# Kernel optimization log

Measured on AMD Instinct MI355X. Metric: run time of the kernel, lower is better.

## Reference

```python
import jax, jax.numpy as jnp
import numpy as np

N_NODES = 8192
N_EDGES = 524288
D_IN = 256
D_OUT = 256


def setup_inputs() -> dict:
    key = jax.random.key(0)
    ks = jax.random.split(key, 8)
    h = jax.random.normal(ks[0], (N_NODES, D_IN), dtype=jnp.float32)
    # Xavier-uniform-like scale for weights
    s = (6.0 / (D_IN + D_OUT)) ** 0.5
    W = jax.random.uniform(ks[1], (D_IN, D_OUT), jnp.float32, -s, s)
    Wq = jax.random.uniform(ks[2], (D_IN, D_OUT), jnp.float32, -s, s)
    bq = jnp.zeros((D_OUT,), jnp.float32)
    Wk = jax.random.uniform(ks[3], (D_IN, D_OUT), jnp.float32, -s, s)
    bk = jnp.zeros((D_OUT,), jnp.float32)
    senders = jax.random.randint(ks[4], (N_EDGES,), 0, N_NODES, dtype=jnp.int64 if jax.config.jax_enable_x64 else jnp.int32)
    receivers = jax.random.randint(ks[5], (N_EDGES,), 0, N_NODES, dtype=jnp.int64 if jax.config.jax_enable_x64 else jnp.int32)
    return {"h": h, "W": W, "Wq": Wq, "bq": bq, "Wk": Wk, "bk": bk,
            "senders": senders, "receivers": receivers}


def reference(h, W, Wq, bq, Wk, bk, senders, receivers):
    # Projected node features: (N, D_OUT)
    h_proj = jnp.dot(h, W)
    # Dense attention logits a = q @ k^T: (N, N), as in the original module
    q = jnp.dot(h, Wq) + bq
    k = jnp.dot(h, Wk) + bk
    a = jnp.dot(q, k.T)
    # Gather per-edge messages and attention weights, weight, scatter-add
    messages = h_proj[senders] * a[senders, receivers][:, None]  # (E, D_OUT)
    aggregated = jax.ops.segment_sum(messages, receivers, num_segments=h.shape[0])
    return jax.nn.relu(aggregated)
```

## Files before the change

kernel.cpp:

```cpp
#include <hip/hip_runtime.h>
#include <stdint.h>

typedef unsigned short u16;
typedef unsigned int u32;
typedef short v8s __attribute__((ext_vector_type(8)));
typedef float v4f __attribute__((ext_vector_type(4)));

#define N_NODES 8192
#define N_EDGES 524288
#define DFEAT 256
#define PAD 160

static __device__ __forceinline__ float bflo(u32 u) { return __uint_as_float(u << 16); }
static __device__ __forceinline__ float bfhi(u32 u) { return __uint_as_float(u & 0xffff0000u); }
static __device__ __forceinline__ u16 f2bf(float f) {
    u32 u = __float_as_uint(f);
    u32 r = (u + 0x7fffu + ((u >> 16) & 1u)) >> 16;
    return (u16)r;
}

__global__ void conv_h(const float* __restrict__ h, u16* __restrict__ hb) {
    int i = (blockIdx.x * 256 + threadIdx.x) * 4;
    float4 v = *(const float4*)(h + i);
    uint2 p;
    p.x = (u32)f2bf(v.x) | ((u32)f2bf(v.y) << 16);
    p.y = (u32)f2bf(v.z) | ((u32)f2bf(v.w) << 16);
    *(uint2*)(hb + i) = p;
}

__global__ void transpose_w(const float* __restrict__ w0, const float* __restrict__ w1,
                            const float* __restrict__ w2, u16* __restrict__ wt) {
    __shared__ u16 t[64][65];
    int b = blockIdx.x;
    int region = b >> 4;
    int tile = b & 15;
    int k0 = (tile >> 2) * 64, n0 = (tile & 3) * 64;
    const float* w = (region == 0) ? w0 : ((region == 1) ? w1 : w2);
    int tx = threadIdx.x & 63, ty = threadIdx.x >> 6;
#pragma unroll
    for (int it = 0; it < 16; it++) {
        int row = it * 4 + ty;
        t[row][tx] = f2bf(w[(k0 + row) * 256 + n0 + tx]);
    }
    __syncthreads();
    u16* o = wt + region * 65536;
#pragma unroll
    for (int it = 0; it < 16; it++) {
        int row = it * 4 + ty;
        o[(n0 + row) * 256 + k0 + tx] = t[tx][row];
    }
}

__global__ void scatter_pad(const int* __restrict__ recv, const int* __restrict__ send,
                            int* __restrict__ cnt, int* __restrict__ es_pad) {
    int e = blockIdx.x * 256 + threadIdx.x;
    int r = recv[e];
    int pos = atomicAdd(&cnt[r], 1);
    if (pos < PAD) es_pad[r * PAD + pos] = send[e];
}

__global__ __launch_bounds__(256) void gemm_proj(
    const u16* __restrict__ h, const u16* __restrict__ wt,
    const float* __restrict__ bq, const float* __restrict__ bk,
    u16* __restrict__ hproj, u16* __restrict__ qb, u16* __restrict__ kb) {
    int wave = threadIdx.x >> 6;
    int lane = threadIdx.x & 63;
    int lm = lane & 15;
    int lq = lane >> 4;
    int m0 = blockIdx.x * 64 + wave * 16;
    int region = blockIdx.y >> 2;
    int n0b = (blockIdx.y & 3) * 64;
    const u16* wtr = wt + region * 65536;

    v4f acc[4];
#pragma unroll
    for (int nt = 0; nt < 4; nt++) acc[nt] = (v4f){0.f, 0.f, 0.f, 0.f};

    const u16* arow = h + (m0 + lm) * 256 + lq * 8;
#pragma unroll
    for (int k0 = 0; k0 < 256; k0 += 32) {
        v8s a = *(const v8s*)(arow + k0);
#pragma unroll
        for (int nt = 0; nt < 4; nt++) {
            v8s b = *(const v8s*)(wtr + (n0b + nt * 16 + lm) * 256 + k0 + lq * 8);
            acc[nt] = __builtin_amdgcn_mfma_f32_16x16x32_bf16(a, b, acc[nt], 0, 0, 0);
        }
    }

    u16* outp = (region == 0) ? hproj : ((region == 1) ? qb : kb);
    const float* bias = (region == 1) ? bq : ((region == 2) ? bk : nullptr);
#pragma unroll
    for (int nt = 0; nt < 4; nt++) {
        int n = n0b + nt * 16 + lm;
        float bv = bias ? bias[n] : 0.f;
#pragma unroll
        for (int i = 0; i < 4; i++) {
            int m = m0 + lq * 4 + i;
            outp[m * 256 + n] = f2bf(acc[nt][i] + bv);
        }
    }
}

__global__ __launch_bounds__(256) void edge_score(
    const u16* __restrict__ qb, const u16* __restrict__ kb,
    const int* __restrict__ cnt, const int* __restrict__ es_pad,
    float* __restrict__ ea_pad) {
    int wave = threadIdx.x >> 6;
    int lane = threadIdx.x & 63;
    int r = blockIdx.x * 4 + wave;
    int lm = lane & 15, lq = lane >> 4;
    int n = min(cnt[r], PAD);
    if (n == 0) return;
    int base = r * PAD;
    const u16* krow = kb + r * 256 + lq * 8;
    for (int c0 = 0; c0 < n; c0 += 16) {
        int j = c0 + lm;
        if (j >= n) j = n - 1;
        int s = es_pad[base + j];
        const u16* qrow = qb + s * 256 + lq * 8;
        v4f acc = (v4f){0.f, 0.f, 0.f, 0.f};
#pragma unroll
        for (int k0 = 0; k0 < 256; k0 += 32) {
            v8s a = *(const v8s*)(qrow + k0);
            v8s bv = *(const v8s*)(krow + k0);
            acc = __builtin_amdgcn_mfma_f32_16x16x32_bf16(a, bv, acc, 0, 0, 0);
        }
        if (lm == 0) {
            float* o = ea_pad + base + c0 + lq * 4;
            o[0] = acc[0]; o[1] = acc[1]; o[2] = acc[2]; o[3] = acc[3];
        }
    }
}

__global__ __launch_bounds__(256) void edge_aggregate(
    const u16* __restrict__ hpb, const int* __restrict__ cnt,
    const int* __restrict__ es_pad, const float* __restrict__ ea_pad,
    float* __restrict__ out) {
    int wave = threadIdx.x >> 6;
    int lane = threadIdx.x & 63;
    int r = blockIdx.x * 4 + wave;
    int n = min(cnt[r], PAD);
    int base = r * PAD;
    int col = lane * 4;
    float a0 = 0.f, a1 = 0.f, a2 = 0.f, a3 = 0.f;
    int i = 0;
    for (; i + 4 <= n; i += 4) {
#pragma unroll
        for (int u = 0; u < 4; u++) {
            int s = es_pad[base + i + u];
            float p = ea_pad[base + i + u];
            uint2 hv = *(const uint2*)(hpb + s * 256 + col);
            a0 += p * bflo(hv.x);
            a1 += p * bfhi(hv.x);
            a2 += p * bflo(hv.y);
            a3 += p * bfhi(hv.y);
        }
    }
    for (; i < n; i++) {
        int s = es_pad[base + i];
        float p = ea_pad[base + i];
        uint2 hv = *(const uint2*)(hpb + s * 256 + col);
        a0 += p * bflo(hv.x);
        a1 += p * bfhi(hv.x);
        a2 += p * bflo(hv.y);
        a3 += p * bfhi(hv.y);
    }
    float4 o;
    o.x = fmaxf(a0, 0.f);
    o.y = fmaxf(a1, 0.f);
    o.z = fmaxf(a2, 0.f);
    o.w = fmaxf(a3, 0.f);
    *(float4*)(out + r * 256 + col) = o;
}

extern "C" void kernel_launch(void* const* d_in, const int* in_sizes, int n_in,
                              void* d_out, int out_size, void* d_ws, size_t ws_size,
                              hipStream_t stream) {
    const float* h  = (const float*)d_in[0];
    const float* W  = (const float*)d_in[1];
    const float* Wq = (const float*)d_in[2];
    const float* bq = (const float*)d_in[3];
    const float* Wk = (const float*)d_in[4];
    const float* bk = (const float*)d_in[5];
    const int* senders   = (const int*)d_in[6];
    const int* receivers = (const int*)d_in[7];
    float* out = (float*)d_out;

    char* ws = (char*)d_ws;
    u16* wt     = (u16*)ws;
    u16* hb     = (u16*)(ws + 393216);
    u16* hproj  = hb + N_NODES * DFEAT;
    u16* qb     = hproj + N_NODES * DFEAT;
    u16* kb     = qb + N_NODES * DFEAT;
    int* cnt    = (int*)(kb + N_NODES * DFEAT);
    int* es_pad = cnt + N_NODES;
    float* ea_pad = (float*)(es_pad + N_NODES * PAD);

    hipMemsetAsync(cnt, 0, N_NODES * sizeof(int), stream);
    conv_h<<<N_NODES * DFEAT / 1024, 256, 0, stream>>>(h, hb);
    transpose_w<<<48, 256, 0, stream>>>(W, Wq, Wk, wt);
    scatter_pad<<<N_EDGES / 256, 256, 0, stream>>>(receivers, senders, cnt, es_pad);
    gemm_proj<<<dim3(128, 12), 256, 0, stream>>>(hb, wt, bq, bk, hproj, qb, kb);
    edge_score<<<N_NODES / 4, 256, 0, stream>>>(qb, kb, cnt, es_pad, ea_pad);
    edge_aggregate<<<N_NODES / 4, 256, 0, stream>>>(hproj, cnt, es_pad, ea_pad, out);
}
```

Baseline: 199.5 us.

## Fuse edge scoring with aggregation and merge prep kernels into one launch

```diff
diff --git a/kernel.cpp b/kernel.cpp
--- a/kernel.cpp
+++ b/kernel.cpp
@@ -19,44 +19,46 @@
     return (u16)r;
 }
 
-__global__ void conv_h(const float* __restrict__ h, u16* __restrict__ hb) {
-    int i = (blockIdx.x * 256 + threadIdx.x) * 4;
-    float4 v = *(const float4*)(h + i);
-    uint2 p;
-    p.x = (u32)f2bf(v.x) | ((u32)f2bf(v.y) << 16);
-    p.y = (u32)f2bf(v.z) | ((u32)f2bf(v.w) << 16);
-    *(uint2*)(hb + i) = p;
-}
-
-__global__ void transpose_w(const float* __restrict__ w0, const float* __restrict__ w1,
-                            const float* __restrict__ w2, u16* __restrict__ wt) {
+__global__ void prep(const float* __restrict__ h,
+                     const float* __restrict__ w0, const float* __restrict__ w1,
+                     const float* __restrict__ w2,
+                     const int* __restrict__ recv, const int* __restrict__ send,
+                     u16* __restrict__ hb, u16* __restrict__ wt,
+                     int* __restrict__ cnt, int* __restrict__ es_pad) {
     __shared__ u16 t[64][65];
     int b = blockIdx.x;
-    int region = b >> 4;
-    int tile = b & 15;
-    int k0 = (tile >> 2) * 64, n0 = (tile & 3) * 64;
-    const float* w = (region == 0) ? w0 : ((region == 1) ? w1 : w2);
-    int tx = threadIdx.x & 63, ty = threadIdx.x >> 6;
-#pragma unroll
-    for (int it = 0; it < 16; it++) {
-        int row = it * 4 + ty;
-        t[row][tx] = f2bf(w[(k0 + row) * 256 + n0 + tx]);
-    }
-    __syncthreads();
-    u16* o = wt + region * 65536;
-#pragma unroll
-    for (int it = 0; it < 16; it++) {
-        int row = it * 4 + ty;
-        o[(n0 + row) * 256 + k0 + tx] = t[tx][row];
-    }
-}
-
-__global__ void scatter_pad(const int* __restrict__ recv, const int* __restrict__ send,
-                            int* __restrict__ cnt, int* __restrict__ es_pad) {
-    int e = blockIdx.x * 256 + threadIdx.x;
-    int r = recv[e];
-    int pos = atomicAdd(&cnt[r], 1);
-    if (pos < PAD) es_pad[r * PAD + pos] = send[e];
+    if (b < 2048) {
+        int i = (b * 256 + threadIdx.x) * 4;
+        float4 v = *(const float4*)(h + i);
+        uint2 p;
+        p.x = (u32)f2bf(v.x) | ((u32)f2bf(v.y) << 16);
+        p.y = (u32)f2bf(v.z) | ((u32)f2bf(v.w) << 16);
+        *(uint2*)(hb + i) = p;
+    } else if (b < 2096) {
+        int bb = b - 2048;
+        int region = bb >> 4;
+        int tile = bb & 15;
+        int k0 = (tile >> 2) * 64, n0 = (tile & 3) * 64;
+        const float* w = (region == 0) ? w0 : ((region == 1) ? w1 : w2);
+        int tx = threadIdx.x & 63, ty = threadIdx.x >> 6;
+#pragma unroll
+        for (int it = 0; it < 16; it++) {
+            int row = it * 4 + ty;
+            t[row][tx] = f2bf(w[(k0 + row) * 256 + n0 + tx]);
+        }
+        __syncthreads();
+        u16* o = wt + region * 65536;
+#pragma unroll
+        for (int it = 0; it < 16; it++) {
+            int row = it * 4 + ty;
+            o[(n0 + row) * 256 + k0 + tx] = t[tx][row];
+        }
+    } else {
+        int e = (b - 2096) * 256 + threadIdx.x;
+        int r = recv[e];
+        int pos = atomicAdd(&cnt[r], 1);
+        if (pos < PAD) es_pad[r * PAD + pos] = send[e];
+    }
 }
 
 __global__ __launch_bounds__(256) void gemm_proj(
@@ -101,18 +103,30 @@
     }
 }
 
-__global__ __launch_bounds__(256) void edge_score(
-    const u16* __restrict__ qb, const u16* __restrict__ kb,
+__global__ __launch_bounds__(256) void edge_fused(
+    const u16* __restrict__ qb, const u16* __restrict__ kb, const u16* __restrict__ hpb,
     const int* __restrict__ cnt, const int* __restrict__ es_pad,
-    float* __restrict__ ea_pad) {
+    float* __restrict__ out) {
+    __shared__ float sc[4][16];
+    __shared__ int   ss[4][16];
     int wave = threadIdx.x >> 6;
     int lane = threadIdx.x & 63;
     int r = blockIdx.x * 4 + wave;
     int lm = lane & 15, lq = lane >> 4;
+    int lh = lane & 31, half = lane >> 5;
+    int colbase = lh * 8;
     int n = min(cnt[r], PAD);
-    if (n == 0) return;
     int base = r * PAD;
+
+    v8s kf[8];
     const u16* krow = kb + r * 256 + lq * 8;
+#pragma unroll
+    for (int t = 0; t < 8; t++) kf[t] = *(const v8s*)(krow + t * 32);
+
+    float a[8];
+#pragma unroll
+    for (int i = 0; i < 8; i++) a[i] = 0.f;
+
     for (int c0 = 0; c0 < n; c0 += 16) {
         int j = c0 + lm;
         if (j >= n) j = n - 1;
@@ -120,57 +134,56 @@
         const u16* qrow = qb + s * 256 + lq * 8;
         v4f acc = (v4f){0.f, 0.f, 0.f, 0.f};
 #pragma unroll
-        for (int k0 = 0; k0 < 256; k0 += 32) {
-            v8s a = *(const v8s*)(qrow + k0);
-            v8s bv = *(const v8s*)(krow + k0);
-            acc = __builtin_amdgcn_mfma_f32_16x16x32_bf16(a, bv, acc, 0, 0, 0);
+        for (int t = 0; t < 8; t++) {
+            v8s av = *(const v8s*)(qrow + t * 32);
+            acc = __builtin_amdgcn_mfma_f32_16x16x32_bf16(av, kf[t], acc, 0, 0, 0);
         }
         if (lm == 0) {
-            float* o = ea_pad + base + c0 + lq * 4;
-            o[0] = acc[0]; o[1] = acc[1]; o[2] = acc[2]; o[3] = acc[3];
-        }
-    }
-}
-
-__global__ __launch_bounds__(256) void edge_aggregate(
-    const u16* __restrict__ hpb, const int* __restrict__ cnt,
-    const int* __restrict__ es_pad, const float* __restrict__ ea_pad,
-    float* __restrict__ out) {
-    int wave = threadIdx.x >> 6;
-    int lane = threadIdx.x & 63;
-    int r = blockIdx.x * 4 + wave;
-    int n = min(cnt[r], PAD);
-    int base = r * PAD;
-    int col = lane * 4;
-    float a0 = 0.f, a1 = 0.f, a2 = 0.f, a3 = 0.f;
-    int i = 0;
-    for (; i + 4 <= n; i += 4) {
-#pragma unroll
-        for (int u = 0; u < 4; u++) {
-            int s = es_pad[base + i + u];
-            float p = ea_pad[base + i + u];
-            uint2 hv = *(const uint2*)(hpb + s * 256 + col);
-            a0 += p * bflo(hv.x);
-            a1 += p * bfhi(hv.x);
-            a2 += p * bflo(hv.y);
-            a3 += p * bfhi(hv.y);
-        }
-    }
-    for (; i < n; i++) {
-        int s = es_pad[base + i];
-        float p = ea_pad[base + i];
-        uint2 hv = *(const uint2*)(hpb + s * 256 + col);
-        a0 += p * bflo(hv.x);
-        a1 += p * bfhi(hv.x);
-        a2 += p * bflo(hv.y);
-        a3 += p * bfhi(hv.y);
-    }
-    float4 o;
-    o.x = fmaxf(a0, 0.f);
-    o.y = fmaxf(a1, 0.f);
-    o.z = fmaxf(a2, 0.f);
-    o.w = fmaxf(a3, 0.f);
-    *(float4*)(out + r * 256 + col) = o;
+#pragma unroll
+            for (int i = 0; i < 4; i++) sc[wave][lq * 4 + i] = acc[i];
+        }
+        if (lq == 0) ss[wave][lm] = s;
+        __threadfence_block();
+
+        int m = n - c0;
+        if (m >= 16) {
+#pragma unroll
+            for (int t0 = 0; t0 < 8; t0++) {
+                int t = t0 * 2 + half;
+                float p = sc[wave][t];
+                int s2 = ss[wave][t];
+                uint4 hv = *(const uint4*)(hpb + s2 * 256 + colbase);
+                a[0] += p * bflo(hv.x); a[1] += p * bfhi(hv.x);
+                a[2] += p * bflo(hv.y); a[3] += p * bfhi(hv.y);
+                a[4] += p * bflo(hv.z); a[5] += p * bfhi(hv.z);
+                a[6] += p * bflo(hv.w); a[7] += p * bfhi(hv.w);
+            }
+        } else {
+            for (int t = half; t < m; t += 2) {
+                float p = sc[wave][t];
+                int s2 = ss[wave][t];
+                uint4 hv = *(const uint4*)(hpb + s2 * 256 + colbase);
+                a[0] += p * bflo(hv.x); a[1] += p * bfhi(hv.x);
+                a[2] += p * bflo(hv.y); a[3] += p * bfhi(hv.y);
+                a[4] += p * bflo(hv.z); a[5] += p * bfhi(hv.z);
+                a[6] += p * bflo(hv.w); a[7] += p * bfhi(hv.w);
+            }
+        }
+    }
+
+#pragma unroll
+    for (int i = 0; i < 8; i++) a[i] += __shfl_xor(a[i], 32, 64);
+
+    if (half == 0) {
+        float4 o0, o1;
+        o0.x = fmaxf(a[0], 0.f); o0.y = fmaxf(a[1], 0.f);
+        o0.z = fmaxf(a[2], 0.f); o0.w = fmaxf(a[3], 0.f);
+        o1.x = fmaxf(a[4], 0.f); o1.y = fmaxf(a[5], 0.f);
+        o1.z = fmaxf(a[6], 0.f); o1.w = fmaxf(a[7], 0.f);
+        float* op = out + r * 256 + colbase;
+        *(float4*)op = o0;
+        *(float4*)(op + 4) = o1;
+    }
 }
 
 extern "C" void kernel_launch(void* const* d_in, const int* in_sizes, int n_in,
@@ -194,13 +207,9 @@
     u16* kb     = qb + N_NODES * DFEAT;
     int* cnt    = (int*)(kb + N_NODES * DFEAT);
     int* es_pad = cnt + N_NODES;
-    float* ea_pad = (float*)(es_pad + N_NODES * PAD);
 
     hipMemsetAsync(cnt, 0, N_NODES * sizeof(int), stream);
-    conv_h<<<N_NODES * DFEAT / 1024, 256, 0, stream>>>(h, hb);
-    transpose_w<<<48, 256, 0, stream>>>(W, Wq, Wk, wt);
-    scatter_pad<<<N_EDGES / 256, 256, 0, stream>>>(receivers, senders, cnt, es_pad);
+    prep<<<4144, 256, 0, stream>>>(h, W, Wq, Wk, receivers, senders, hb, wt, cnt, es_pad);
     gemm_proj<<<dim3(128, 12), 256, 0, stream>>>(hb, wt, bq, bk, hproj, qb, kb);
-    edge_score<<<N_NODES / 4, 256, 0, stream>>>(qb, kb, cnt, es_pad, ea_pad);
-    edge_aggregate<<<N_NODES / 4, 256, 0, stream>>>(hproj, cnt, es_pad, ea_pad, out);
-}
+    edge_fused<<<N_NODES / 4, 256, 0, stream>>>(qb, kb, hproj, cnt, es_pad, out);
+}
```

Result: faster. 182.2 us (-8.7%).
